# Optimization experiments

Measured on AMD Instinct MI355X. Metric: run time of the kernel, lower is better.

## Reference

```python
import jax, jax.numpy as jnp
import numpy as np
import math

N_HEADS = 32
N_KV_HEADS = 8
HEAD_DIM = 64
ROPE_BASE = 10000.0


def _rope_cos_sin(L, dtype):
    # inv_freq: [head_dim/2]
    inv_freq = 1.0 / (ROPE_BASE ** (jnp.arange(0, HEAD_DIM, 2, dtype=jnp.float32) / HEAD_DIM))
    t = jnp.arange(L, dtype=jnp.float32)
    freqs = jnp.outer(t, inv_freq)            # [L, head_dim/2]
    emb = jnp.concatenate([freqs, freqs], -1)  # [L, head_dim]
    return jnp.cos(emb).astype(dtype), jnp.sin(emb).astype(dtype)


def _rotate_half(x):
    x1, x2 = jnp.split(x, 2, axis=-1)
    return jnp.concatenate([-x2, x1], axis=-1)


def setup_inputs() -> dict:
    key = jax.random.key(0)
    ks = jax.random.split(key, 5)
    B, L, D = 2, 2048, 2048
    s = 0.02
    return {
        "x": jax.random.normal(ks[0], (B, L, D), jnp.float32),
        "Wq": jax.random.normal(ks[1], (D, N_HEADS * HEAD_DIM), jnp.float32) * s,
        "Wk": jax.random.normal(ks[2], (D, N_KV_HEADS * HEAD_DIM), jnp.float32) * s,
        "Wv": jax.random.normal(ks[3], (D, N_KV_HEADS * HEAD_DIM), jnp.float32) * s,
        "Wo": jax.random.normal(ks[4], (N_HEADS * HEAD_DIM, D), jnp.float32) * s,
    }


def reference(x, Wq, Wk, Wv, Wo):
    B, L, D = x.shape
    G = N_HEADS // N_KV_HEADS
    # QKV projections -> [B, H, L, hd]
    q = (x @ Wq).reshape(B, L, N_HEADS, HEAD_DIM).transpose(0, 2, 1, 3)
    k = (x @ Wk).reshape(B, L, N_KV_HEADS, HEAD_DIM).transpose(0, 2, 1, 3)
    v = (x @ Wv).reshape(B, L, N_KV_HEADS, HEAD_DIM).transpose(0, 2, 1, 3)
    # RoPE
    cos, sin = _rope_cos_sin(L, x.dtype)  # [L, hd]
    cos = cos[None, None]
    sin = sin[None, None]
    q = q * cos + _rotate_half(q) * sin
    k = k * cos + _rotate_half(k) * sin
    # GQA expand kv heads (repeat_interleave along head dim)
    k = jnp.repeat(k, G, axis=1)
    v = jnp.repeat(v, G, axis=1)
    # Causal SDPA
    scale = 1.0 / math.sqrt(HEAD_DIM)
    scores = jnp.einsum('bhqd,bhkd->bhqk', q, k) * scale  # [B,H,L,L]
    causal = jnp.tril(jnp.ones((L, L), bool))
    scores = jnp.where(causal[None, None], scores, jnp.finfo(scores.dtype).min)
    probs = jax.nn.softmax(scores, axis=-1)
    out = jnp.einsum('bhqk,bhkd->bhqd', probs, v)  # [B,H,L,hd]
    out = out.transpose(0, 2, 1, 3).reshape(B, L, N_HEADS * HEAD_DIM)
    return out @ Wo
```

## Files before the change

### kernel.cpp

```cpp
#include <hip/hip_runtime.h>
#include <hip/hip_bf16.h>
#include <stdint.h>

typedef __bf16 bf16_t;
typedef bf16_t bf16x2 __attribute__((ext_vector_type(2)));
typedef bf16_t bf16x4 __attribute__((ext_vector_type(4)));
typedef bf16_t bf16x8 __attribute__((ext_vector_type(8)));
typedef float f32x4 __attribute__((ext_vector_type(4)));
typedef float f32x16 __attribute__((ext_vector_type(16)));

#define NH 32
#define NKV 8
#define HD 64
#define LSEQ 2048
#define DMODEL 2048
#define BATCH 2

#define QSCALE 0.18033688011112042f
#define FIXED_M 12.0f

__device__ __forceinline__ void gl_lds16(const void* g, void* l) {
  __builtin_amdgcn_global_load_lds(
      (__attribute__((address_space(1))) char*)(uintptr_t)g,
      (__attribute__((address_space(3))) char*)(uintptr_t)l, 16, 0, 0);
}

__device__ __forceinline__ unsigned pack2(float a, float b) {
  bf16x2 t;
  t[0] = (bf16_t)a;
  t[1] = (bf16_t)b;
  return __builtin_bit_cast(unsigned, t);
}


__global__ void cvt_x(const float4* __restrict__ s, bf16x4* __restrict__ d, int n4) {
  int i = blockIdx.x * blockDim.x + threadIdx.x;
  if (i >= n4) return;
  float4 v = s[i];
  bf16x4 o;
  o[0] = (bf16_t)v.x; o[1] = (bf16_t)v.y; o[2] = (bf16_t)v.z; o[3] = (bf16_t)v.w;
  d[i] = o;
}

__global__ void transpose_w(const float* __restrict__ W, bf16_t* __restrict__ WT,
                            int K, int N) {
  __shared__ float tile[32][33];
  int nb = blockIdx.x * 32, kb = blockIdx.y * 32;
  int tx = threadIdx.x, ty = threadIdx.y;
#pragma unroll
  for (int i = 0; i < 32; i += 8)
    tile[ty + i][tx] = W[(size_t)(kb + ty + i) * N + nb + tx];
  __syncthreads();
#pragma unroll
  for (int i = 0; i < 32; i += 8)
    WT[(size_t)(nb + ty + i) * K + kb + tx] = (bf16_t)tile[tx][ty + i];
}

__global__ void rope_table(float* __restrict__ cosT, float* __restrict__ sinT) {
  int t = blockIdx.x * blockDim.x + threadIdx.x;
  int l = t >> 5, i = t & 31;
  float inv = powf(10000.0f, -(float)i / 32.0f);
  float ang = (float)l * inv;
  float s, c;
  sincosf(ang, &s, &c);
  cosT[t] = c;
  sinT[t] = s;
}

template <int EPI>
__global__ __launch_bounds__(256, 3) void gemm128(
    const bf16_t* __restrict__ A, const bf16_t* __restrict__ BT,
    float* __restrict__ Cf, bf16_t* __restrict__ Qo, bf16_t* __restrict__ Ko,
    bf16_t* __restrict__ Vo, int M, int N, int K,
    const float* __restrict__ cosT, const float* __restrict__ sinT, int nx) {
  __shared__ bf16_t Al[128 * 64];
  __shared__ bf16_t Bl[128 * 64];
  const int tid = threadIdx.x, lane = tid & 63, w = tid >> 6;
  const int wm = w >> 1, wn = w & 1;
  const int r15 = lane & 15, g = lane >> 4;
  const int nwg = (int)gridDim.x;
  const int sid = ((int)blockIdx.x & 7) * (nwg >> 3) + ((int)blockIdx.x >> 3);
  const int m0 = (sid / nx) * 128, n0 = (sid % nx) * 128;
  f32x4 acc[4][4] = {};

  for (int kt = 0; kt < K; kt += 64) {
#pragma unroll
    for (int i = 0; i < 4; ++i) {
      const int c = i * 256 + tid;
      const int row = c >> 3, cc = c & 7;
      const int sc = (cc ^ (row & 7)) * 8;
      gl_lds16(A + (size_t)(m0 + row) * K + kt + sc, Al + c * 8);
      gl_lds16(BT + (size_t)(n0 + row) * K + kt + sc, Bl + c * 8);
    }
    __syncthreads();
#pragma unroll
    for (int kk = 0; kk < 2; ++kk) {
      bf16x8 af[4], bfr[4];
#pragma unroll
      for (int mi = 0; mi < 4; ++mi) {
        const int r = wm * 64 + mi * 16 + r15;
        af[mi] = *(const bf16x8*)((const char*)Al + r * 128 +
                                  (((kk * 4 + g) ^ (r & 7)) << 4));
      }
#pragma unroll
      for (int ni = 0; ni < 4; ++ni) {
        const int r = wn * 64 + ni * 16 + r15;
        bfr[ni] = *(const bf16x8*)((const char*)Bl + r * 128 +
                                   (((kk * 4 + g) ^ (r & 7)) << 4));
      }
#pragma unroll
      for (int mi = 0; mi < 4; ++mi)
#pragma unroll
        for (int ni = 0; ni < 4; ++ni)
          acc[mi][ni] = __builtin_amdgcn_mfma_f32_16x16x32_bf16(
              af[mi], bfr[ni], acc[mi][ni], 0, 0, 0);
    }
    __syncthreads();
  }

  if constexpr (EPI == 0) {
#pragma unroll
    for (int mi = 0; mi < 4; ++mi) {
      const int row = m0 + wm * 64 + mi * 16 + g * 4;
#pragma unroll
      for (int ni = 0; ni < 4; ++ni) {
        const int col = n0 + wn * 64 + ni * 16 + r15;
#pragma unroll
        for (int r = 0; r < 4; ++r)
          Cf[(size_t)(row + r) * N + col] = acc[mi][ni][r];
      }
    }
  } else {
    const int colbase = n0 + wn * 64;
    auto rope_store = [&](bf16_t* C, int NHT, int colrel, float sc) {
#pragma unroll
      for (int mi = 0; mi < 4; ++mi)
#pragma unroll
        for (int r = 0; r < 4; ++r) {
          const int rowg = m0 + wm * 64 + mi * 16 + g * 4 + r;
          const int bb = rowg >> 11, ls = rowg & (LSEQ - 1);
#pragma unroll
          for (int ni = 0; ni < 2; ++ni) {
            const int col = colrel + ni * 16 + r15;
            const int hh = col >> 6, d = col & 63;
            const float c = cosT[ls * 32 + d], s = sinT[ls * 32 + d];
            const float v0 = acc[mi][ni][r], v1 = acc[mi][ni + 2][r];
            bf16_t* dst = C + (((size_t)bb * NHT + hh) * LSEQ + ls) * HD + d;
            dst[0] = (bf16_t)((v0 * c - v1 * s) * sc);
            dst[32] = (bf16_t)((v1 * c + v0 * s) * sc);
          }
        }
    };
    if (n0 < 2048) {
      rope_store(Qo, NH, colbase, QSCALE);
    } else if (n0 < 2560) {
      rope_store(Ko, NKV, colbase - 2048, 1.0f);
    } else {
#pragma unroll
      for (int mi = 0; mi < 4; ++mi)
#pragma unroll
        for (int r = 0; r < 4; ++r) {
          const int rowg = m0 + wm * 64 + mi * 16 + g * 4 + r;
          const int bb = rowg >> 11, ls = rowg & (LSEQ - 1);
#pragma unroll
          for (int ni = 0; ni < 4; ++ni) {
            const int col = colbase - 2560 + ni * 16 + r15;
            const int hh = col >> 6, d = col & 63;
            Vo[(((size_t)bb * NKV + hh) * HD + d) * LSEQ + ls] =
                (bf16_t)acc[mi][ni][r];
          }
        }
    }
  }
}

__global__ __launch_bounds__(512, 4) void attn_fwd(
    const bf16_t* __restrict__ Q, const bf16_t* __restrict__ Kh,
    const bf16_t* __restrict__ VTh, bf16_t* __restrict__ AO) {
  __shared__ bf16_t Kl[2][64 * 64];
  __shared__ bf16_t Vl[2][64 * 64];
  const int tid = threadIdx.x, lane = tid & 63, w = tid >> 6;
  const int col = lane & 31, hi = lane >> 5;
  const int hk = (int)blockIdx.x & 7, b = (int)blockIdx.x >> 3;
  const int a = (int)blockIdx.y & 15, k = (int)blockIdx.y >> 4;
  const int qt = k ? 31 - a : a;
  const int h = hk * 4 + (w & 3);
  const int qoff = (w >> 2) * 32;

  const bf16_t* Qb =
      Q + (((size_t)b * NH + h) * LSEQ + (size_t)qt * 64 + qoff) * HD;
  const bf16_t* Kb = Kh + ((size_t)b * NKV + hk) * LSEQ * HD;
  const bf16_t* Vb = VTh + ((size_t)b * NKV + hk) * HD * LSEQ;

  const int nt = qt + 1;

  bf16x8 ones8;
#pragma unroll
  for (int j = 0; j < 8; ++j) ones8[j] = (bf16_t)1.0f;

  auto stage = [&](int buf, int kt) {
    const int row = tid >> 3, cc = tid & 7;
    const int scol = (cc ^ (row & 7)) * 16;
    gl_lds16((const char*)Kb + (size_t)(kt * 64 + row) * 128 + scol,
             (char*)&Kl[buf][0] + tid * 16);
    gl_lds16((const char*)Vb + (size_t)row * 4096 + (size_t)kt * 128 + scol,
             (char*)&Vl[buf][0] + tid * 16);
  };

  bf16x8 qf[4];
#pragma unroll
  for (int kc = 0; kc < 4; ++kc)
    qf[kc] = *(const bf16x8*)&Qb[(size_t)col * HD + kc * 16 + hi * 8];

  f32x16 o[2] = {};
  f32x16 osum = {};

  int cur = 0;
  stage(cur, 0);
  __syncthreads();
  for (int kt = 0; kt < nt; ++kt) {
    if (kt + 1 < nt) stage(cur ^ 1, kt + 1);
    const bool diag = (kt == nt - 1);
    const char* Kcur = (const char*)&Kl[cur][0];
    const char* Vcur = (const char*)&Vl[cur][0];

    f32x16 sfrag[2] = {};
#pragma unroll
    for (int kvs = 0; kvs < 2; ++kvs) {
      if (diag && kvs * 32 > 31 + qoff) {
#pragma unroll
        for (int r = 0; r < 16; ++r) sfrag[kvs][r] = -1e30f;
        continue;
      }
      bf16x8 ak[4];
#pragma unroll
      for (int kc = 0; kc < 4; ++kc) {
        const int row = kvs * 32 + col;
        const int slot = ((kc * 2 + hi) ^ (row & 7)) * 16;
        ak[kc] = *(const bf16x8*)(Kcur + row * 128 + slot);
      }
#pragma unroll
      for (int kc = 0; kc < 4; ++kc)
        sfrag[kvs] = __builtin_amdgcn_mfma_f32_32x32x16_bf16(
            ak[kc], qf[kc], sfrag[kvs], 0, 0, 0);
    }

    if (diag) {
#pragma unroll
      for (int kvs = 0; kvs < 2; ++kvs)
#pragma unroll
        for (int r = 0; r < 16; ++r) {
          const int kvl = kvs * 32 + (r & 3) + 8 * (r >> 2) + 4 * hi;
          if (kvl > col + qoff) sfrag[kvs][r] = -1e30f;
        }
    }

    bf16x8 pf[4];
#pragma unroll
    for (int kvs = 0; kvs < 2; ++kvs)
#pragma unroll
      for (int c1 = 0; c1 < 2; ++c1) {
        float pv[8];
#pragma unroll
        for (int j = 0; j < 8; ++j)
          pv[j] = __builtin_amdgcn_exp2f(sfrag[kvs][c1 * 8 + j] - FIXED_M);
        const unsigned a01 = pack2(pv[0], pv[1]), a23 = pack2(pv[2], pv[3]);
        const unsigned b01 = pack2(pv[4], pv[5]), b23 = pack2(pv[6], pv[7]);
        const unsigned s01 = __shfl_xor(hi ? a01 : b01, 32);
        const unsigned s23 = __shfl_xor(hi ? a23 : b23, 32);
        union { unsigned u[4]; bf16x8 v; } t;
        t.u[0] = hi ? s01 : a01;
        t.u[1] = hi ? s23 : a23;
        t.u[2] = hi ? b01 : s01;
        t.u[3] = hi ? b23 : s23;
        pf[kvs * 2 + c1] = t.v;
      }

#pragma unroll
    for (int ds = 0; ds < 2; ++ds) {
      bf16x8 av[4];
#pragma unroll
      for (int kc2 = 0; kc2 < 4; ++kc2) {
        const int row = ds * 32 + col;
        const int slot = ((kc2 * 2 + hi) ^ (row & 7)) * 16;
        av[kc2] = *(const bf16x8*)(Vcur + row * 128 + slot);
      }
#pragma unroll
      for (int kc2 = 0; kc2 < 4; ++kc2) {
        if (diag && kc2 * 16 > 31 + qoff) continue;
        o[ds] = __builtin_amdgcn_mfma_f32_32x32x16_bf16(
            av[kc2], pf[kc2], o[ds], 0, 0, 0);
      }
    }
#pragma unroll
    for (int kc2 = 0; kc2 < 4; ++kc2) {
      if (diag && kc2 * 16 > 31 + qoff) continue;
      osum = __builtin_amdgcn_mfma_f32_32x32x16_bf16(
          ones8, pf[kc2], osum, 0, 0, 0);
    }

    __syncthreads();
    cur ^= 1;
  }

  const float inv = 1.0f / osum[0];
  const int q = qt * 64 + qoff + col;
#pragma unroll
  for (int ds = 0; ds < 2; ++ds)
#pragma unroll
    for (int g4 = 0; g4 < 4; ++g4) {
      bf16x4 o4;
#pragma unroll
      for (int j = 0; j < 4; ++j) o4[j] = (bf16_t)(o[ds][g4 * 4 + j] * inv);
      const int d = ds * 32 + 8 * g4 + 4 * hi;
      *(bf16x4*)&AO[((size_t)b * LSEQ + q) * DMODEL + h * HD + d] = o4;
    }
}


extern "C" void kernel_launch(void* const* d_in, const int* in_sizes, int n_in,
                              void* d_out, int out_size, void* d_ws, size_t ws_size,
                              hipStream_t stream) {
  const float* x = (const float*)d_in[0];
  const float* Wq = (const float*)d_in[1];
  const float* Wk = (const float*)d_in[2];
  const float* Wv = (const float*)d_in[3];
  const float* Wo = (const float*)d_in[4];
  char* ws = (char*)d_ws;
  size_t off = 0;
  auto alloc = [&](size_t bytes) {
    char* p = ws + off;
    off += (bytes + 255) & ~(size_t)255;
    return p;
  };
  bf16_t* xb = (bf16_t*)alloc((size_t)BATCH * LSEQ * DMODEL * 2);
  bf16_t* wqkvT = (bf16_t*)alloc((size_t)3072 * DMODEL * 2);
  bf16_t* wot = (bf16_t*)alloc((size_t)DMODEL * DMODEL * 2);
  float* cosT = (float*)alloc((size_t)LSEQ * 32 * 4);
  float* sinT = (float*)alloc((size_t)LSEQ * 32 * 4);
  bf16_t* Qh = (bf16_t*)alloc((size_t)BATCH * NH * LSEQ * HD * 2);
  bf16_t* Kh = (bf16_t*)alloc((size_t)BATCH * NKV * LSEQ * HD * 2);
  bf16_t* VTh = (bf16_t*)alloc((size_t)BATCH * NKV * HD * LSEQ * 2);
  bf16_t* AO = (bf16_t*)alloc((size_t)BATCH * LSEQ * NH * HD * 2);
  (void)ws_size; (void)in_sizes; (void)n_in; (void)out_size;

  const int M = BATCH * LSEQ;

  cvt_x<<<(M * DMODEL / 4 + 255) / 256, 256, 0, stream>>>(
      (const float4*)x, (bf16x4*)xb, M * DMODEL / 4);
  transpose_w<<<dim3(64, 64), dim3(32, 8), 0, stream>>>(Wq, wqkvT, 2048, 2048);
  transpose_w<<<dim3(16, 64), dim3(32, 8), 0, stream>>>(
      Wk, wqkvT + (size_t)2048 * 2048, 2048, 512);
  transpose_w<<<dim3(16, 64), dim3(32, 8), 0, stream>>>(
      Wv, wqkvT + (size_t)2560 * 2048, 2048, 512);
  transpose_w<<<dim3(64, 64), dim3(32, 8), 0, stream>>>(Wo, wot, 2048, 2048);
  rope_table<<<LSEQ * 32 / 256, 256, 0, stream>>>(cosT, sinT);

  gemm128<3><<<768, 256, 0, stream>>>(
      xb, wqkvT, nullptr, Qh, Kh, VTh, M, 3072, 2048, cosT, sinT, 24);

  attn_fwd<<<dim3(16, 32), 512, 0, stream>>>(Qh, Kh, VTh, AO);

  gemm128<0><<<512, 256, 0, stream>>>(
      AO, wot, (float*)d_out, nullptr, nullptr, nullptr, M, 2048, 2048,
      nullptr, nullptr, 16);
}
```

Measured before the change: 174.1 us.

## Replace 128x128 GEMM with double-buffered 256-row tile pipelined GEMM

```diff
diff --git a/kernel.cpp b/kernel.cpp
--- a/kernel.cpp
+++ b/kernel.cpp
@@ -67,64 +67,110 @@
   sinT[t] = s;
 }
 
-template <int EPI>
-__global__ __launch_bounds__(256, 3) void gemm128(
+template <int EPI, int NREP>
+__global__ __launch_bounds__(512, 1) void gemm256(
     const bf16_t* __restrict__ A, const bf16_t* __restrict__ BT,
     float* __restrict__ Cf, bf16_t* __restrict__ Qo, bf16_t* __restrict__ Ko,
     bf16_t* __restrict__ Vo, int M, int N, int K,
     const float* __restrict__ cosT, const float* __restrict__ sinT, int nx) {
-  __shared__ bf16_t Al[128 * 64];
-  __shared__ bf16_t Bl[128 * 64];
+  constexpr int BN = NREP * 64;
+  __shared__ bf16_t Al[2][4 * 4096];
+  __shared__ bf16_t Bl[2][NREP * 4096];
   const int tid = threadIdx.x, lane = tid & 63, w = tid >> 6;
-  const int wm = w >> 1, wn = w & 1;
+  const int wm = w >> 2, wn = w & 3;
   const int r15 = lane & 15, g = lane >> 4;
   const int nwg = (int)gridDim.x;
   const int sid = ((int)blockIdx.x & 7) * (nwg >> 3) + ((int)blockIdx.x >> 3);
-  const int m0 = (sid / nx) * 128, n0 = (sid % nx) * 128;
-  f32x4 acc[4][4] = {};
-
-  for (int kt = 0; kt < K; kt += 64) {
-#pragma unroll
-    for (int i = 0; i < 4; ++i) {
-      const int c = i * 256 + tid;
-      const int row = c >> 3, cc = c & 7;
-      const int sc = (cc ^ (row & 7)) * 8;
-      gl_lds16(A + (size_t)(m0 + row) * K + kt + sc, Al + c * 8);
-      gl_lds16(BT + (size_t)(n0 + row) * K + kt + sc, Bl + c * 8);
-    }
-    __syncthreads();
-#pragma unroll
-    for (int kk = 0; kk < 2; ++kk) {
-      bf16x8 af[4], bfr[4];
-#pragma unroll
-      for (int mi = 0; mi < 4; ++mi) {
-        const int r = wm * 64 + mi * 16 + r15;
-        af[mi] = *(const bf16x8*)((const char*)Al + r * 128 +
-                                  (((kk * 4 + g) ^ (r & 7)) << 4));
-      }
-#pragma unroll
-      for (int ni = 0; ni < 4; ++ni) {
-        const int r = wn * 64 + ni * 16 + r15;
-        bfr[ni] = *(const bf16x8*)((const char*)Bl + r * 128 +
-                                   (((kk * 4 + g) ^ (r & 7)) << 4));
-      }
-#pragma unroll
-      for (int mi = 0; mi < 4; ++mi)
-#pragma unroll
-        for (int ni = 0; ni < 4; ++ni)
-          acc[mi][ni] = __builtin_amdgcn_mfma_f32_16x16x32_bf16(
-              af[mi], bfr[ni], acc[mi][ni], 0, 0, 0);
-    }
-    __syncthreads();
+  const int m0 = (sid / nx) * 256, n0 = (sid % nx) * BN;
+
+  f32x4 acc[8][NREP] = {};
+
+  const int NT = K >> 6;
+  const int NI = NT >> 1;
+
+  auto stage_q = [&](bf16_t* dst, const bf16_t* src, int row0, int kt) {
+    const int r = tid >> 3;
+    const int sc = (((tid & 7) ^ (r & 7)) << 3);
+    gl_lds16(src + (size_t)(row0 + r) * K + (kt << 6) + sc, dst + tid * 8);
+  };
+  auto stage_step = [&](int d, int kt, int s) {
+    kt = kt < NT ? kt : NT - 1;
+    if (NREP == 4) {
+      if (s == 0) { stage_q(&Bl[d][0], BT, n0, kt); stage_q(&Bl[d][4096], BT, n0 + 64, kt); }
+      else if (s == 1) { stage_q(&Bl[d][8192], BT, n0 + 128, kt); stage_q(&Bl[d][12288], BT, n0 + 192, kt); }
+      else if (s == 2) { stage_q(&Al[d][0], A, m0, kt); stage_q(&Al[d][8192], A, m0 + 128, kt); }
+      else { stage_q(&Al[d][4096], A, m0 + 64, kt); stage_q(&Al[d][12288], A, m0 + 192, kt); }
+    } else {
+      if (s == 0) { stage_q(&Bl[d][0], BT, n0, kt); stage_q(&Bl[d][4096], BT, n0 + 64, kt); }
+      else if (s == 1) { stage_q(&Al[d][0], A, m0, kt); stage_q(&Al[d][8192], A, m0 + 128, kt); }
+      else if (s == 2) { stage_q(&Al[d][4096], A, m0 + 64, kt); stage_q(&Al[d][12288], A, m0 + 192, kt); }
+    }
+  };
+  auto lda = [&](int d, int mi, int kk) -> bf16x8 {
+    const int ar = (wm << 7) + (mi << 4) + r15;
+    return *(const bf16x8*)((const char*)&Al[d][(ar >> 6) << 12] +
+                            (ar & 63) * 128 + ((((kk << 2) + g) ^ (ar & 7)) << 4));
+  };
+  auto ldb = [&](int d, int ni, int kk) -> bf16x8 {
+    const int br = wn * (NREP << 4) + (ni << 4) + r15;
+    return *(const bf16x8*)((const char*)&Bl[d][(br >> 6) << 12] +
+                            (br & 63) * 128 + ((((kk << 2) + g) ^ (br & 7)) << 4));
+  };
+
+  stage_step(0, 0, 0);
+  stage_step(0, 0, 1);
+  stage_step(0, 0, 2);
+  stage_step(0, 0, 3);
+
+  for (int i = 0; i < NI; ++i) {
+#pragma unroll
+    for (int hf = 0; hf < 2; ++hf) {
+      const int dC = hf;
+      const int dS = hf ^ 1;
+      const int ktS = (i << 1) + 1 + hf;
+      bf16x8 bf0[NREP][2];
+#pragma unroll
+      for (int q = 0; q < 4; ++q) {
+        stage_step(dS, ktS, q);
+        if (q == 0) asm volatile("s_waitcnt vmcnt(4)" ::: "memory");
+        if (q == 2) asm volatile("s_waitcnt vmcnt(6)" ::: "memory");
+        __builtin_amdgcn_s_barrier();
+        asm volatile("" ::: "memory");
+        if (q == 0) {
+#pragma unroll
+          for (int ni = 0; ni < NREP; ++ni)
+#pragma unroll
+            for (int kk = 0; kk < 2; ++kk) bf0[ni][kk] = ldb(dC, ni, kk);
+        }
+        bf16x8 af[2][2];
+#pragma unroll
+        for (int t2 = 0; t2 < 2; ++t2)
+#pragma unroll
+          for (int kk = 0; kk < 2; ++kk) af[t2][kk] = lda(dC, 2 * q + t2, kk);
+        __builtin_amdgcn_s_setprio(1);
+#pragma unroll
+        for (int t2 = 0; t2 < 2; ++t2)
+#pragma unroll
+          for (int ni = 0; ni < NREP; ++ni)
+#pragma unroll
+            for (int kk = 0; kk < 2; ++kk)
+              acc[2 * q + t2][ni] = __builtin_amdgcn_mfma_f32_16x16x32_bf16(
+                  af[t2][kk], bf0[ni][kk], acc[2 * q + t2][ni], 0, 0, 0);
+        __builtin_amdgcn_s_setprio(0);
+        asm volatile("" ::: "memory");
+        __builtin_amdgcn_s_barrier();
+      }
+    }
   }
+  asm volatile("s_waitcnt vmcnt(0)" ::: "memory");
 
   if constexpr (EPI == 0) {
 #pragma unroll
-    for (int mi = 0; mi < 4; ++mi) {
-      const int row = m0 + wm * 64 + mi * 16 + g * 4;
-#pragma unroll
-      for (int ni = 0; ni < 4; ++ni) {
-        const int col = n0 + wn * 64 + ni * 16 + r15;
+    for (int mi = 0; mi < 8; ++mi) {
+      const int row = m0 + wm * 128 + mi * 16 + g * 4;
+#pragma unroll
+      for (int ni = 0; ni < NREP; ++ni) {
+        const int col = n0 + wn * (NREP * 16) + ni * 16 + r15;
 #pragma unroll
         for (int r = 0; r < 4; ++r)
           Cf[(size_t)(row + r) * N + col] = acc[mi][ni][r];
@@ -134,10 +180,10 @@
     const int colbase = n0 + wn * 64;
     auto rope_store = [&](bf16_t* C, int NHT, int colrel, float sc) {
 #pragma unroll
-      for (int mi = 0; mi < 4; ++mi)
+      for (int mi = 0; mi < 8; ++mi)
 #pragma unroll
         for (int r = 0; r < 4; ++r) {
-          const int rowg = m0 + wm * 64 + mi * 16 + g * 4 + r;
+          const int rowg = m0 + wm * 128 + mi * 16 + g * 4 + r;
           const int bb = rowg >> 11, ls = rowg & (LSEQ - 1);
 #pragma unroll
           for (int ni = 0; ni < 2; ++ni) {
@@ -157,10 +203,10 @@
       rope_store(Ko, NKV, colbase - 2048, 1.0f);
     } else {
 #pragma unroll
-      for (int mi = 0; mi < 4; ++mi)
+      for (int mi = 0; mi < 8; ++mi)
 #pragma unroll
         for (int r = 0; r < 4; ++r) {
-          const int rowg = m0 + wm * 64 + mi * 16 + g * 4 + r;
+          const int rowg = m0 + wm * 128 + mi * 16 + g * 4 + r;
           const int bb = rowg >> 11, ls = rowg & (LSEQ - 1);
 #pragma unroll
           for (int ni = 0; ni < 4; ++ni) {
@@ -356,12 +402,12 @@
   transpose_w<<<dim3(64, 64), dim3(32, 8), 0, stream>>>(Wo, wot, 2048, 2048);
   rope_table<<<LSEQ * 32 / 256, 256, 0, stream>>>(cosT, sinT);
 
-  gemm128<3><<<768, 256, 0, stream>>>(
-      xb, wqkvT, nullptr, Qh, Kh, VTh, M, 3072, 2048, cosT, sinT, 24);
+  gemm256<3, 4><<<192, 512, 0, stream>>>(
+      xb, wqkvT, nullptr, Qh, Kh, VTh, M, 3072, 2048, cosT, sinT, 12);
 
   attn_fwd<<<dim3(16, 32), 512, 0, stream>>>(Qh, Kh, VTh, AO);
 
-  gemm128<0><<<512, 256, 0, stream>>>(
+  gemm256<0, 2><<<256, 512, 0, stream>>>(
       AO, wot, (float*)d_out, nullptr, nullptr, nullptr, M, 2048, 2048,
       nullptr, nullptr, 16);
 }
```

Result: no change. 173.8 us (-0.2%).
